# Kernel tuning notes

Hardware: AMD Instinct MI355X
Metric: run time of the kernel (lower is better)

Reference implementation:

```python
import jax, jax.numpy as jnp
import numpy as np

B = 4          # documents per batch
L = 128        # unique candidate entity links
S = 2048       # predicted spans (max over batch)
N = 1 + L + S  # root + links + spans


def setup_inputs() -> dict:
    key = jax.random.key(0)
    k1, k2, k3 = jax.random.split(key, 3)
    # coref/linking edge scores over [root | links | spans] x [root | links | spans]
    scores = jax.random.normal(k1, (B, N, N), dtype=jnp.float32) * 0.1
    eye = jnp.eye(N, dtype=jnp.float32)
    # z mask: all admissible edges -- no self loops, no incoming edges to root
    z_mask = jnp.ones((B, N, N), dtype=jnp.float32) * (1.0 - eye)[None]
    z_mask = z_mask.at[:, :, 0].set(0.0)
    # target mask: sparse subset of z edges + root->all so a spanning
    # arborescence always exists (mirrors the gold cluster / gold link edges)
    tgt = (jax.random.uniform(k2, (B, N, N)) < 0.05).astype(jnp.float32) * z_mask
    tgt = tgt.at[:, 0, 1:].set(1.0)
    # ragged valid lengths per batch element (1 + unique_links_len + n_pred_spans)
    lengths = jnp.array([N, N - 256, N - 512, N - 64], dtype=jnp.int32)
    return {"scores": scores, "target_mask": tgt, "z_mask": z_mask, "lengths": lengths}


def _mtt_log_partition(scores, mask, lengths):
    """Matrix-tree theorem log-partition: logdet of the root-minor of the
    Laplacian of exp(scores) restricted to edges in `mask` and to the first
    `lengths[b]` nodes of each batch element."""
    n = scores.shape[-1]
    valid = (jnp.arange(n)[None, :] < lengths[:, None]).astype(scores.dtype)  # [B,N]
    w = jnp.exp(scores) * mask * valid[:, :, None] * valid[:, None, :]        # [B,N,N]
    colsum = jnp.sum(w, axis=-2)                                              # incoming weight per node
    lap = colsum[:, :, None] * jnp.eye(n, dtype=scores.dtype)[None] - w       # L = D_in - W
    minor = lap[:, 1:, 1:]                                                    # drop root row/col
    # pad the diagonal of invalid (past-length) nodes with 1 so they
    # contribute logdet 0 instead of making the minor singular
    pad = 1.0 - valid[:, 1:]
    minor = minor + pad[:, :, None] * jnp.eye(n - 1, dtype=scores.dtype)[None]
    _, logdet = jnp.linalg.slogdet(minor)
    return logdet


def reference(scores, target_mask, z_mask, lengths):
    log_z = _mtt_log_partition(scores, z_mask, lengths)        # log partition over all arborescences
    log_t = _mtt_log_partition(scores, target_mask, lengths)   # log weight of gold arborescences
    return jnp.mean(log_z - log_t)                             # MTT negative log-likelihood
```

## Files before the change

kernel.cpp:

```cpp
#include <hip/hip_runtime.h>
#include <math.h>

#define NFULL 2177
#define NN    2176
#define NB    64
#define NMAT  8
#define NBATCH 4


__global__ void init_cs_kernel(float* __restrict__ cs) {
  int i = blockIdx.x * blockDim.x + threadIdx.x;
  if (i < NMAT * NN) cs[i] = 0.f;
}

__global__ void colsum_kernel(const float* __restrict__ scores,
                              const float* __restrict__ zm,
                              const float* __restrict__ tm,
                              const int* __restrict__ lengths,
                              float* __restrict__ cs) {
  int c = blockIdx.x * blockDim.x + threadIdx.x;
  if (c >= NN) return;
  int rc = blockIdx.y;
  int b  = blockIdx.z;
  int len = lengths[b];
  int j = c + 1;
  if (j >= len) return;
  int i0 = rc * 128;
  int i1 = i0 + 128; if (i1 > len) i1 = len;
  if (i0 >= i1) return;
  size_t base = (size_t)b * NFULL * NFULL + j;
  float az = 0.f, at = 0.f;
  for (int i = i0; i < i1; ++i) {
    size_t off = base + (size_t)i * NFULL;
    float e = __expf(scores[off]);
    az += e * zm[off];
    at += e * tm[off];
  }
  atomicAdd(&cs[b * NN + c], az);
  atomicAdd(&cs[(NBATCH + b) * NN + c], at);
}

__global__ void build_kernel(const float* __restrict__ scores,
                             const float* __restrict__ zm,
                             const float* __restrict__ tm,
                             const int* __restrict__ lengths,
                             const float* __restrict__ cs,
                             float* __restrict__ M) {
  int c = blockIdx.x * blockDim.x + threadIdx.x;
  if (c >= NN) return;
  int r = blockIdx.y;
  int b = blockIdx.z;
  int len = lengths[b];
  int i = r + 1, j = c + 1;
  float vz = 0.f, vt = 0.f;
  if (i < len && j < len) {
    size_t off = (size_t)b * NFULL * NFULL + (size_t)i * NFULL + j;
    float e = __expf(scores[off]);
    vz = e * zm[off];
    vt = e * tm[off];
  }
  float dz = 0.f, dt = 0.f;
  if (r == c) {
    float pad = (j < len) ? 0.f : 1.f;
    dz = cs[b * NN + c] + pad;
    dt = cs[(NBATCH + b) * NN + c] + pad;
  }
  size_t mo = (size_t)r * NN + c;
  M[(size_t)b * NN * NN + mo]            = dz - vz;
  M[(size_t)(NBATCH + b) * NN * NN + mo] = dt - vt;
}


__global__ __launch_bounds__(256) void factor_diag(float* __restrict__ Mb, int k0) {
  __shared__ float T[64][65];
  int m = blockIdx.x;
  float* A = Mb + (size_t)m * NN * NN;
  int tid = threadIdx.x;
  for (int idx = tid; idx < 64 * 64; idx += 256) {
    int r = idx >> 6, c = idx & 63;
    T[r][c] = A[(size_t)(k0 + r) * NN + (k0 + c)];
  }
  __syncthreads();
  for (int j = 0; j < 63; ++j) {
    float inv = 1.0f / T[j][j];
    for (int r = j + 1 + tid; r < 64; r += 256) T[r][j] *= inv;
    __syncthreads();
    int rem = 63 - j;
    for (int idx = tid; idx < rem * rem; idx += 256) {
      int rr = j + 1 + idx / rem;
      int cc = j + 1 + idx % rem;
      T[rr][cc] -= T[rr][j] * T[j][cc];
    }
    __syncthreads();
  }
  for (int idx = tid; idx < 64 * 64; idx += 256) {
    int r = idx >> 6, c = idx & 63;
    A[(size_t)(k0 + r) * NN + (k0 + c)] = T[r][c];
  }
}

__global__ __launch_bounds__(64) void panel_solve(float* __restrict__ Mb, int k0) {
  __shared__ float D[64][65];
  __shared__ float T[64][65];
  int m    = blockIdx.y;
  int role = blockIdx.z;
  float* A = Mb + (size_t)m * NN * NN;
  int tid = threadIdx.x;
  int obase = k0 + 64 + blockIdx.x * 64;
  for (int idx = tid; idx < 64 * 64; idx += 64) {
    int r = idx >> 6, c = idx & 63;
    D[r][c] = A[(size_t)(k0 + r) * NN + (k0 + c)];
  }
  if (role == 0) {
    for (int idx = tid; idx < 64 * 64; idx += 64) {
      int r = idx >> 6, c = idx & 63;
      T[r][c] = A[(size_t)(obase + r) * NN + (k0 + c)];
    }
    __syncthreads();
    for (int j = 0; j < 64; ++j) {
      float acc = T[tid][j];
      for (int t = 0; t < j; ++t) acc -= T[tid][t] * D[t][j];
      T[tid][j] = acc / D[j][j];
    }
    __syncthreads();
    for (int idx = tid; idx < 64 * 64; idx += 64) {
      int r = idx >> 6, c = idx & 63;
      A[(size_t)(obase + r) * NN + (k0 + c)] = T[r][c];
    }
  } else {
    for (int idx = tid; idx < 64 * 64; idx += 64) {
      int r = idx >> 6, c = idx & 63;
      T[r][c] = A[(size_t)(k0 + r) * NN + (obase + c)];
    }
    __syncthreads();
    int c = tid;
    for (int j = 1; j < 64; ++j) {
      float acc = T[j][c];
      for (int t = 0; t < j; ++t) acc -= D[j][t] * T[t][c];
      T[j][c] = acc;
    }
    __syncthreads();
    for (int idx = tid; idx < 64 * 64; idx += 64) {
      int r = idx >> 6, c = idx & 63;
      A[(size_t)(k0 + r) * NN + (obase + c)] = T[r][c];
    }
  }
}

__global__ __launch_bounds__(256) void trail_gemm(float* __restrict__ Mb, int k0) {
  __shared__ float Lt[64][68];
  __shared__ float Ut[64][68];
  int m = blockIdx.z;
  float* A = Mb + (size_t)m * NN * NN;
  int base  = k0 + 64;
  int rbase = base + blockIdx.y * 64;
  int cbase = base + blockIdx.x * 64;
  int tid = threadIdx.x;
  for (int idx = tid; idx < 64 * 64; idx += 256) {
    int r = idx >> 6, k = idx & 63;
    Lt[k][r] = A[(size_t)(rbase + r) * NN + (k0 + k)];
  }
  for (int idx = tid; idx < 64 * 64; idx += 256) {
    int k = idx >> 6, c = idx & 63;
    Ut[k][c] = A[(size_t)(k0 + k) * NN + (cbase + c)];
  }
  __syncthreads();
  int c0 = (tid & 15) << 2;
  int r0 = (tid >> 4) << 2;
  float acc[4][4];
#pragma unroll
  for (int i = 0; i < 4; ++i)
#pragma unroll
    for (int jj = 0; jj < 4; ++jj) acc[i][jj] = 0.f;
#pragma unroll 8
  for (int k = 0; k < 64; ++k) {
    float4 a  = *(const float4*)&Lt[k][r0];
    float4 bv = *(const float4*)&Ut[k][c0];
    acc[0][0] += a.x * bv.x; acc[0][1] += a.x * bv.y; acc[0][2] += a.x * bv.z; acc[0][3] += a.x * bv.w;
    acc[1][0] += a.y * bv.x; acc[1][1] += a.y * bv.y; acc[1][2] += a.y * bv.z; acc[1][3] += a.y * bv.w;
    acc[2][0] += a.z * bv.x; acc[2][1] += a.z * bv.y; acc[2][2] += a.z * bv.z; acc[2][3] += a.z * bv.w;
    acc[3][0] += a.w * bv.x; acc[3][1] += a.w * bv.y; acc[3][2] += a.w * bv.z; acc[3][3] += a.w * bv.w;
  }
#pragma unroll
  for (int i = 0; i < 4; ++i) {
    float4* p = (float4*)&A[(size_t)(rbase + r0 + i) * NN + (cbase + c0)];
    float4 v = *p;
    v.x -= acc[i][0]; v.y -= acc[i][1]; v.z -= acc[i][2]; v.w -= acc[i][3];
    *p = v;
  }
}


__global__ void logdet_kernel(const float* __restrict__ Mb, double* __restrict__ dlog) {
  int m = blockIdx.x;
  const float* A = Mb + (size_t)m * NN * NN;
  double s = 0.0;
  for (int i = threadIdx.x; i < NN; i += 256)
    s += (double)logf(fabsf(A[(size_t)i * NN + i]));
  __shared__ double red[256];
  red[threadIdx.x] = s;
  __syncthreads();
  for (int k = 128; k > 0; k >>= 1) {
    if (threadIdx.x < k) red[threadIdx.x] += red[threadIdx.x + k];
    __syncthreads();
  }
  if (threadIdx.x == 0) dlog[m] = red[0];
}

__global__ void final_kernel(const double* __restrict__ dlog, float* __restrict__ out) {
  if (threadIdx.x == 0) {
    double acc = 0.0;
    for (int b = 0; b < NBATCH; ++b) acc += dlog[b] - dlog[NBATCH + b];
    out[0] = (float)(acc * 0.25);
  }
}


extern "C" void kernel_launch(void* const* d_in, const int* in_sizes, int n_in,
                              void* d_out, int out_size, void* d_ws, size_t ws_size,
                              hipStream_t stream) {
  const float* scores  = (const float*)d_in[0];
  const float* tm      = (const float*)d_in[1];
  const float* zm      = (const float*)d_in[2];
  const int*   lengths = (const int*)d_in[3];
  float* out = (float*)d_out;

  float* M  = (float*)d_ws;
  float* cs = M + (size_t)NMAT * NN * NN;
  double* dlog = (double*)(cs + (size_t)NMAT * NN);

  init_cs_kernel<<<(NMAT * NN + 255) / 256, 256, 0, stream>>>(cs);
  colsum_kernel<<<dim3((NN + 255) / 256, (NFULL + 127) / 128, NBATCH), 256, 0, stream>>>(
      scores, zm, tm, lengths, cs);
  build_kernel<<<dim3((NN + 255) / 256, NN, NBATCH), 256, 0, stream>>>(
      scores, zm, tm, lengths, cs, M);

  for (int k0 = 0; k0 < NN; k0 += NB) {
    factor_diag<<<NMAT, 256, 0, stream>>>(M, k0);
    int rem = NN - k0 - NB;
    if (rem > 0) {
      panel_solve<<<dim3(rem / 64, NMAT, 2), 64, 0, stream>>>(M, k0);
      trail_gemm<<<dim3(rem / 64, rem / 64, NMAT), 256, 0, stream>>>(M, k0);
    }
  }

  logdet_kernel<<<NMAT, 256, 0, stream>>>(M, dlog);
  final_kernel<<<1, 64, 0, stream>>>(dlog, out);
}
```

Measured before the change: 4.511 ms.

## Fuse colsum into build, enlarge LU tiles, fold next diag factor into GEMM

Merges the column-sum and matrix-build passes into one kernel that streams scores once and writes the off-diagonal Laplacian, with a small diag-fix kernel that adds the column sums afterward. The trailing GEMM now uses 128x128 tiles with an 8x8 register block and swizzled shared memory, and panel solves handle 128 rows or columns per block. The factorization of the next 64x64 diagonal block is done inside the (0,0) trailing GEMM block, which removes one launch per step. This cuts the number of launches and the global traffic, but serializes the diagonal factor onto a single block per matrix and raises register pressure.

New measurement: 5.281 ms. +17.1%, slower.

```diff
diff --git a/kernel.cpp b/kernel.cpp
--- a/kernel.cpp
+++ b/kernel.cpp
@@ -3,7 +3,6 @@
 
 #define NFULL 2177
 #define NN    2176
-#define NB    64
 #define NMAT  8
 #define NBATCH 4
 
@@ -13,180 +12,243 @@
   if (i < NMAT * NN) cs[i] = 0.f;
 }
 
-__global__ void colsum_kernel(const float* __restrict__ scores,
-                              const float* __restrict__ zm,
-                              const float* __restrict__ tm,
-                              const int* __restrict__ lengths,
-                              float* __restrict__ cs) {
-  int c = blockIdx.x * blockDim.x + threadIdx.x;
+__global__ __launch_bounds__(256) void build_kernel(
+    const float* __restrict__ scores, const float* __restrict__ zm,
+    const float* __restrict__ tm, const int* __restrict__ lengths,
+    float* __restrict__ M, float* __restrict__ cs) {
+  int c = blockIdx.x * 256 + threadIdx.x;
   if (c >= NN) return;
-  int rc = blockIdx.y;
-  int b  = blockIdx.z;
+  int b = blockIdx.z;
   int len = lengths[b];
   int j = c + 1;
-  if (j >= len) return;
-  int i0 = rc * 128;
-  int i1 = i0 + 128; if (i1 > len) i1 = len;
-  if (i0 >= i1) return;
-  size_t base = (size_t)b * NFULL * NFULL + j;
+  bool jv = (j < len);
+  int r0 = blockIdx.y * 16;
+  size_t sbase = (size_t)b * NFULL * NFULL;
+  float* Mz = M + (size_t)b * NN * NN;
+  float* Mt = M + (size_t)(NBATCH + b) * NN * NN;
   float az = 0.f, at = 0.f;
-  for (int i = i0; i < i1; ++i) {
-    size_t off = base + (size_t)i * NFULL;
-    float e = __expf(scores[off]);
-    az += e * zm[off];
-    at += e * tm[off];
+  for (int rr = 0; rr < 16; ++rr) {
+    int r = r0 + rr, i = r + 1;
+    float vz = 0.f, vt = 0.f;
+    if (jv && i < len) {
+      size_t off = sbase + (size_t)i * NFULL + j;
+      float e = __expf(scores[off]);
+      vz = e * zm[off];
+      vt = e * tm[off];
+    }
+    Mz[(size_t)r * NN + c] = -vz;
+    Mt[(size_t)r * NN + c] = -vt;
+    az += vz; at += vt;
   }
   atomicAdd(&cs[b * NN + c], az);
   atomicAdd(&cs[(NBATCH + b) * NN + c], at);
 }
 
-__global__ void build_kernel(const float* __restrict__ scores,
-                             const float* __restrict__ zm,
-                             const float* __restrict__ tm,
-                             const int* __restrict__ lengths,
-                             const float* __restrict__ cs,
-                             float* __restrict__ M) {
-  int c = blockIdx.x * blockDim.x + threadIdx.x;
+__global__ void diag_fix_kernel(const float* __restrict__ scores,
+                                const float* __restrict__ zm,
+                                const float* __restrict__ tm,
+                                const int* __restrict__ lengths,
+                                const float* __restrict__ cs,
+                                float* __restrict__ M) {
+  int c = blockIdx.x * 256 + threadIdx.x;
   if (c >= NN) return;
-  int r = blockIdx.y;
-  int b = blockIdx.z;
+  int m = blockIdx.y;
+  int b = m & 3;
+  const float* msk = (m < NBATCH) ? zm : tm;
   int len = lengths[b];
-  int i = r + 1, j = c + 1;
-  float vz = 0.f, vt = 0.f;
-  if (i < len && j < len) {
-    size_t off = (size_t)b * NFULL * NFULL + (size_t)i * NFULL + j;
-    float e = __expf(scores[off]);
-    vz = e * zm[off];
-    vt = e * tm[off];
-  }
-  float dz = 0.f, dt = 0.f;
-  if (r == c) {
-    float pad = (j < len) ? 0.f : 1.f;
-    dz = cs[b * NN + c] + pad;
-    dt = cs[(NBATCH + b) * NN + c] + pad;
-  }
-  size_t mo = (size_t)r * NN + c;
-  M[(size_t)b * NN * NN + mo]            = dz - vz;
-  M[(size_t)(NBATCH + b) * NN * NN + mo] = dt - vt;
-}
-
+  int j = c + 1;
+  float w0 = 0.f, pad = 1.f;
+  if (j < len) {
+    size_t off = (size_t)b * NFULL * NFULL + j;
+    w0 = __expf(scores[off]) * msk[off];
+    pad = 0.f;
+  }
+  M[(size_t)m * NN * NN + (size_t)c * NN + c] = cs[m * NN + c] + w0 + pad;
+}
+
+
+__device__ inline void factor64_lds(float* D, int tid) {
+  for (int j = 0; j < 63; ++j) {
+    float inv = 1.0f / D[j * 65 + j];
+    for (int r = j + 1 + tid; r < 64; r += 256) D[r * 65 + j] *= inv;
+    __syncthreads();
+    int cc = j + 1 + (tid & 63);
+    for (int rr = j + 1 + (tid >> 6); rr < 64; rr += 4) {
+      if (cc < 64) D[rr * 65 + cc] -= D[rr * 65 + j] * D[j * 65 + cc];
+    }
+    __syncthreads();
+  }
+}
 
 __global__ __launch_bounds__(256) void factor_diag(float* __restrict__ Mb, int k0) {
-  __shared__ float T[64][65];
+  __shared__ float D[64 * 65];
   int m = blockIdx.x;
   float* A = Mb + (size_t)m * NN * NN;
   int tid = threadIdx.x;
   for (int idx = tid; idx < 64 * 64; idx += 256) {
     int r = idx >> 6, c = idx & 63;
-    T[r][c] = A[(size_t)(k0 + r) * NN + (k0 + c)];
+    D[r * 65 + c] = A[(size_t)(k0 + r) * NN + k0 + c];
   }
   __syncthreads();
-  for (int j = 0; j < 63; ++j) {
-    float inv = 1.0f / T[j][j];
-    for (int r = j + 1 + tid; r < 64; r += 256) T[r][j] *= inv;
-    __syncthreads();
-    int rem = 63 - j;
-    for (int idx = tid; idx < rem * rem; idx += 256) {
-      int rr = j + 1 + idx / rem;
-      int cc = j + 1 + idx % rem;
-      T[rr][cc] -= T[rr][j] * T[j][cc];
-    }
-    __syncthreads();
-  }
+  factor64_lds(D, tid);
   for (int idx = tid; idx < 64 * 64; idx += 256) {
     int r = idx >> 6, c = idx & 63;
-    A[(size_t)(k0 + r) * NN + (k0 + c)] = T[r][c];
-  }
-}
-
-__global__ __launch_bounds__(64) void panel_solve(float* __restrict__ Mb, int k0) {
-  __shared__ float D[64][65];
-  __shared__ float T[64][65];
-  int m    = blockIdx.y;
-  int role = blockIdx.z;
+    A[(size_t)(k0 + r) * NN + k0 + c] = D[r * 65 + c];
+  }
+}
+
+__global__ __launch_bounds__(128) void panel_solve(float* __restrict__ Mb, int k0) {
+  __shared__ float D[64 * 65];
+  __shared__ float invD[64];
+  __shared__ float T[128 * 67];
+  int m = blockIdx.y, role = blockIdx.z;
   float* A = Mb + (size_t)m * NN * NN;
   int tid = threadIdx.x;
-  int obase = k0 + 64 + blockIdx.x * 64;
-  for (int idx = tid; idx < 64 * 64; idx += 64) {
+  int rem = NN - k0 - 64;
+  int sbase = blockIdx.x * 128;
+  for (int idx = tid; idx < 64 * 64; idx += 128) {
     int r = idx >> 6, c = idx & 63;
-    D[r][c] = A[(size_t)(k0 + r) * NN + (k0 + c)];
-  }
+    D[r * 65 + c] = A[(size_t)(k0 + r) * NN + k0 + c];
+  }
+  __syncthreads();
+  if (tid < 64) invD[tid] = 1.0f / D[tid * 65 + tid];
   if (role == 0) {
-    for (int idx = tid; idx < 64 * 64; idx += 64) {
+    int nrow = rem - sbase; if (nrow > 128) nrow = 128;
+    for (int idx = tid; idx < 128 * 64; idx += 128) {
       int r = idx >> 6, c = idx & 63;
-      T[r][c] = A[(size_t)(obase + r) * NN + (k0 + c)];
-    }
-    __syncthreads();
-    for (int j = 0; j < 64; ++j) {
-      float acc = T[tid][j];
-      for (int t = 0; t < j; ++t) acc -= T[tid][t] * D[t][j];
-      T[tid][j] = acc / D[j][j];
-    }
-    __syncthreads();
-    for (int idx = tid; idx < 64 * 64; idx += 64) {
+      if (r < nrow) T[r * 67 + c] = A[(size_t)(k0 + 64 + sbase + r) * NN + k0 + c];
+    }
+    __syncthreads();
+    if (tid < nrow) {
+      float* Tr = &T[tid * 67];
+      for (int j = 0; j < 64; ++j) {
+        float acc = Tr[j];
+        for (int t = 0; t < j; ++t) acc -= Tr[t] * D[t * 65 + j];
+        Tr[j] = acc * invD[j];
+      }
+    }
+    __syncthreads();
+    for (int idx = tid; idx < 128 * 64; idx += 128) {
       int r = idx >> 6, c = idx & 63;
-      A[(size_t)(obase + r) * NN + (k0 + c)] = T[r][c];
+      if (r < nrow) A[(size_t)(k0 + 64 + sbase + r) * NN + k0 + c] = T[r * 67 + c];
     }
   } else {
-    for (int idx = tid; idx < 64 * 64; idx += 64) {
-      int r = idx >> 6, c = idx & 63;
-      T[r][c] = A[(size_t)(k0 + r) * NN + (obase + c)];
-    }
-    __syncthreads();
-    int c = tid;
-    for (int j = 1; j < 64; ++j) {
-      float acc = T[j][c];
-      for (int t = 0; t < j; ++t) acc -= D[j][t] * T[t][c];
-      T[j][c] = acc;
-    }
-    __syncthreads();
-    for (int idx = tid; idx < 64 * 64; idx += 64) {
-      int r = idx >> 6, c = idx & 63;
-      A[(size_t)(k0 + r) * NN + (obase + c)] = T[r][c];
+    int ncol = rem - sbase; if (ncol > 128) ncol = 128;
+    for (int idx = tid; idx < 64 * 128; idx += 128) {
+      int r = idx >> 7, c = idx & 127;
+      if (c < ncol) T[r * 130 + c] = A[(size_t)(k0 + r) * NN + k0 + 64 + sbase + c];
+    }
+    __syncthreads();
+    if (tid < ncol) {
+      for (int j = 1; j < 64; ++j) {
+        float acc = T[j * 130 + tid];
+        for (int t = 0; t < j; ++t) acc -= D[j * 65 + t] * T[t * 130 + tid];
+        T[j * 130 + tid] = acc;
+      }
+    }
+    __syncthreads();
+    for (int idx = tid; idx < 64 * 128; idx += 128) {
+      int r = idx >> 7, c = idx & 127;
+      if (c < ncol) A[(size_t)(k0 + r) * NN + k0 + 64 + sbase + c] = T[r * 130 + c];
     }
   }
 }
 
 __global__ __launch_bounds__(256) void trail_gemm(float* __restrict__ Mb, int k0) {
-  __shared__ float Lt[64][68];
-  __shared__ float Ut[64][68];
+  __shared__ float La[128 * 64];
+  __shared__ float Ub[64 * 128];
   int m = blockIdx.z;
   float* A = Mb + (size_t)m * NN * NN;
-  int base  = k0 + 64;
-  int rbase = base + blockIdx.y * 64;
-  int cbase = base + blockIdx.x * 64;
+  int base = k0 + 64;
+  int rbase = base + blockIdx.y * 128;
+  int cbase = base + blockIdx.x * 128;
   int tid = threadIdx.x;
-  for (int idx = tid; idx < 64 * 64; idx += 256) {
-    int r = idx >> 6, k = idx & 63;
-    Lt[k][r] = A[(size_t)(rbase + r) * NN + (k0 + k)];
-  }
-  for (int idx = tid; idx < 64 * 64; idx += 256) {
-    int k = idx >> 6, c = idx & 63;
-    Ut[k][c] = A[(size_t)(k0 + k) * NN + (cbase + c)];
+#pragma unroll
+  for (int it = 0; it < 8; ++it) {
+    int idx = tid + it * 256;
+    int r = idx >> 4, k4 = idx & 15;
+    int gr = rbase + r; if (gr >= NN) gr = NN - 1;
+    float4 v = *(const float4*)&A[(size_t)gr * NN + k0 + k4 * 4];
+    int sw = (k4 ^ ((r >> 2) & 3)) * 4;
+    *(float4*)&La[r * 64 + sw] = v;
+  }
+#pragma unroll
+  for (int it = 0; it < 8; ++it) {
+    int idx = tid + it * 256;
+    int k = idx >> 5, c4 = idx & 31;
+    int gc = cbase + c4 * 4;
+    float4 v = make_float4(0.f, 0.f, 0.f, 0.f);
+    if (gc + 3 < NN) v = *(const float4*)&A[(size_t)(k0 + k) * NN + gc];
+    *(float4*)&Ub[k * 128 + c4 * 4] = v;
   }
   __syncthreads();
-  int c0 = (tid & 15) << 2;
-  int r0 = (tid >> 4) << 2;
-  float acc[4][4];
-#pragma unroll
-  for (int i = 0; i < 4; ++i)
-#pragma unroll
-    for (int jj = 0; jj < 4; ++jj) acc[i][jj] = 0.f;
-#pragma unroll 8
-  for (int k = 0; k < 64; ++k) {
-    float4 a  = *(const float4*)&Lt[k][r0];
-    float4 bv = *(const float4*)&Ut[k][c0];
-    acc[0][0] += a.x * bv.x; acc[0][1] += a.x * bv.y; acc[0][2] += a.x * bv.z; acc[0][3] += a.x * bv.w;
-    acc[1][0] += a.y * bv.x; acc[1][1] += a.y * bv.y; acc[1][2] += a.y * bv.z; acc[1][3] += a.y * bv.w;
-    acc[2][0] += a.z * bv.x; acc[2][1] += a.z * bv.y; acc[2][2] += a.z * bv.z; acc[2][3] += a.z * bv.w;
-    acc[3][0] += a.w * bv.x; acc[3][1] += a.w * bv.y; acc[3][2] += a.w * bv.z; acc[3][3] += a.w * bv.w;
-  }
-#pragma unroll
-  for (int i = 0; i < 4; ++i) {
-    float4* p = (float4*)&A[(size_t)(rbase + r0 + i) * NN + (cbase + c0)];
-    float4 v = *p;
-    v.x -= acc[i][0]; v.y -= acc[i][1]; v.z -= acc[i][2]; v.w -= acc[i][3];
-    *p = v;
+  int r0 = (tid >> 4) * 4;
+  int c0 = (tid & 15) * 4;
+  float acc[8][8];
+#pragma unroll
+  for (int i = 0; i < 8; ++i)
+#pragma unroll
+    for (int jj = 0; jj < 8; ++jj) acc[i][jj] = 0.f;
+#pragma unroll 2
+  for (int kc = 0; kc < 16; ++kc) {
+    float4 av[8], bv[8];
+#pragma unroll
+    for (int i = 0; i < 4; ++i) {
+      int r = r0 + i;
+      int sw = (kc ^ ((r >> 2) & 3)) * 4;
+      av[i]     = *(const float4*)&La[r * 64 + sw];
+      av[4 + i] = *(const float4*)&La[(r + 64) * 64 + sw];
+    }
+#pragma unroll
+    for (int kk = 0; kk < 4; ++kk) {
+      bv[2 * kk]     = *(const float4*)&Ub[(kc * 4 + kk) * 128 + c0];
+      bv[2 * kk + 1] = *(const float4*)&Ub[(kc * 4 + kk) * 128 + c0 + 64];
+    }
+#pragma unroll
+    for (int kk = 0; kk < 4; ++kk) {
+      float bc[8];
+      bc[0] = ((const float*)&bv[2 * kk])[0];     bc[1] = ((const float*)&bv[2 * kk])[1];
+      bc[2] = ((const float*)&bv[2 * kk])[2];     bc[3] = ((const float*)&bv[2 * kk])[3];
+      bc[4] = ((const float*)&bv[2 * kk + 1])[0]; bc[5] = ((const float*)&bv[2 * kk + 1])[1];
+      bc[6] = ((const float*)&bv[2 * kk + 1])[2]; bc[7] = ((const float*)&bv[2 * kk + 1])[3];
+#pragma unroll
+      for (int i = 0; i < 8; ++i) {
+        float aval = ((const float*)&av[i])[kk];
+#pragma unroll
+        for (int jj = 0; jj < 8; ++jj) acc[i][jj] += aval * bc[jj];
+      }
+    }
+  }
+#pragma unroll
+  for (int i = 0; i < 8; ++i) {
+    int row = rbase + r0 + (i < 4 ? i : 60 + i);
+    if (row < NN) {
+#pragma unroll
+      for (int h = 0; h < 2; ++h) {
+        int col = cbase + c0 + h * 64;
+        if (col < NN) {
+          float4* p = (float4*)&A[(size_t)row * NN + col];
+          float4 v = *p;
+          v.x -= acc[i][h * 4 + 0]; v.y -= acc[i][h * 4 + 1];
+          v.z -= acc[i][h * 4 + 2]; v.w -= acc[i][h * 4 + 3];
+          *p = v;
+        }
+      }
+    }
+  }
+  if (blockIdx.x == 0 && blockIdx.y == 0) {
+    __syncthreads();
+    float* D = La;
+    for (int idx = tid; idx < 64 * 64; idx += 256) {
+      int r = idx >> 6, c = idx & 63;
+      D[r * 65 + c] = A[(size_t)(base + r) * NN + base + c];
+    }
+    __syncthreads();
+    factor64_lds(D, tid);
+    for (int idx = tid; idx < 64 * 64; idx += 256) {
+      int r = idx >> 6, c = idx & 63;
+      A[(size_t)(base + r) * NN + base + c] = D[r * 65 + c];
+    }
   }
 }
 
@@ -230,18 +292,17 @@
   double* dlog = (double*)(cs + (size_t)NMAT * NN);
 
   init_cs_kernel<<<(NMAT * NN + 255) / 256, 256, 0, stream>>>(cs);
-  colsum_kernel<<<dim3((NN + 255) / 256, (NFULL + 127) / 128, NBATCH), 256, 0, stream>>>(
-      scores, zm, tm, lengths, cs);
-  build_kernel<<<dim3((NN + 255) / 256, NN, NBATCH), 256, 0, stream>>>(
+  build_kernel<<<dim3((NN + 255) / 256, NN / 16, NBATCH), 256, 0, stream>>>(
+      scores, zm, tm, lengths, M, cs);
+  diag_fix_kernel<<<dim3((NN + 255) / 256, NMAT), 256, 0, stream>>>(
       scores, zm, tm, lengths, cs, M);
-
-  for (int k0 = 0; k0 < NN; k0 += NB) {
-    factor_diag<<<NMAT, 256, 0, stream>>>(M, k0);
-    int rem = NN - k0 - NB;
-    if (rem > 0) {
-      panel_solve<<<dim3(rem / 64, NMAT, 2), 64, 0, stream>>>(M, k0);
-      trail_gemm<<<dim3(rem / 64, rem / 64, NMAT), 256, 0, stream>>>(M, k0);
-    }
+  factor_diag<<<NMAT, 256, 0, stream>>>(M, 0);
+
+  for (int k0 = 0; k0 < NN - 64; k0 += 64) {
+    int rem = NN - k0 - 64;
+    int nt = (rem + 127) / 128;
+    panel_solve<<<dim3(nt, NMAT, 2), 128, 0, stream>>>(M, k0);
+    trail_gemm<<<dim3(nt, nt, NMAT), 256, 0, stream>>>(M, k0);
   }
 
   logdet_kernel<<<NMAT, 256, 0, stream>>>(M, dlog);
```
